# Optimization experiments

Hardware: AMD Instinct MI355X
Metric: run time of the kernel (lower is better)

Reference implementation:

```python
import jax, jax.numpy as jnp
import numpy as np

SAMPLERATE = 22050
N_OCTAVES = 16
N_SAMPLES = 32768
MIN_FREQ = 20.0 / (SAMPLERATE // 2)
MAX_FREQ = 3000.0 / (SAMPLERATE // 2)
FREQ_RANGE = MAX_FREQ - MIN_FREQ
BASE_RESONANCE = 0.01


def max_norm(x, axis=-1, eps=1e-8):
    return x / (jnp.max(jnp.abs(x), axis=axis, keepdims=True) + eps)


def exponential_decay(decay_values, n_octaves):
    # decay_values: (B, E, 1). Note the original applies sigmoid here on top of
    # the sigmoid already applied in forward (sigmoid_decay=True) -> double sigmoid.
    dv = jax.nn.sigmoid(decay_values)  # (B, E, 1)
    resonance_factor = (1.0 - BASE_RESONANCE) * 0.99
    decay = BASE_RESONANCE + dv * resonance_factor  # (B, E, 1)
    logd = jnp.log(decay + 1e-12)
    b, e, _ = decay_values.shape
    # cumsum of a per-(b,e) constant over octaves, then exp (matches torch code;
    # F.interpolate to size==n_octaves is the identity here)
    logd = jnp.broadcast_to(logd, (b, e, n_octaves))
    return jnp.exp(jnp.cumsum(logd, axis=-1))  # (B, E, O)


def setup_inputs() -> dict:
    key = jax.random.key(0)
    k1, k2, k3 = jax.random.split(key, 3)
    B, E = 8, 64
    return {
        "f0": jax.random.uniform(k1, (B, E, 1), dtype=jnp.float32),
        "decay_coefficients": jax.random.normal(k2, (B, E, 1), dtype=jnp.float32),
        "unused": jnp.zeros((B, E, 1), dtype=jnp.float32),
        "freq_spacing": jax.random.uniform(k3, (B, E, 1), dtype=jnp.float32),
    }


def reference(f0, decay_coefficients, unused, freq_spacing):
    b, e, _ = f0.shape
    O, S = N_OCTAVES, N_SAMPLES

    f0 = jnp.abs(f0)  # (B, E, 1)
    # sigmoid_decay=True path: sigmoid applied before exponential_decay
    exp_decays = exponential_decay(jax.nn.sigmoid(decay_coefficients), O)  # (B, E, O)

    f0 = (MIN_FREQ + f0 * FREQ_RANGE) * jnp.pi  # (B, E, 1)

    # freq_spacing repeated over octaves then cumsum -> per-octave factors
    factors = jnp.cumsum(jnp.broadcast_to(freq_spacing, (b, e, O)), axis=-1)
    f0s = f0 * factors  # (B, E, O)

    # nyquist cutoff
    f0s = f0s * (f0s < 1.0)

    # phase: cumsum over samples of constant per-octave frequency (faithful to torch)
    phase = jnp.cumsum(jnp.broadcast_to(f0s[..., None], (b, e, O, S)), axis=-1)
    osc = jnp.sin(phase)  # (B, E, O, S)

    osc = osc * exp_decays[..., None]
    osc = jnp.sum(osc, axis=2)  # (B, E, S)
    return max_norm(osc, axis=-1)
```

## Files before the change

### kernel.cpp

```cpp
#include <hip/hip_runtime.h>
#include <hip/hip_fp16.h>
#include <math.h>

#define N_OCT 16
#define NPAIR 8
#define NS    32768
#define TPB   512
#define SPT   (NS / TPB)
#define N_BE  512

typedef float v2f __attribute__((ext_vector_type(2)));
typedef _Float16 h4 __attribute__((ext_vector_type(4)));

static __device__ __forceinline__ v2f fma2(v2f a, v2f b, v2f c) {
    return __builtin_elementwise_fma(a, b, c);
}

__global__ __launch_bounds__(TPB, 4)
void f0res_kernel(const float* __restrict__ f0_in,
                  const float* __restrict__ dc_in,
                  const float* __restrict__ fs_in,
                  float* __restrict__ out)
{
    extern __shared__ _Float16 smem[];
    __shared__ float wmax[TPB / 64];

    const int be = blockIdx.x;
    const int t  = threadIdx.x;

    const float f0a = fabsf(f0_in[be]);
    const float dc  = dc_in[be];
    const float fs  = fs_in[be];

    const float MINF = (float)(20.0 / 11025.0);
    const float FRNG = (float)(3000.0 / 11025.0 - 20.0 / 11025.0);

    const float s1    = 1.0f / (1.0f + __expf(-dc));
    const float dv    = 1.0f / (1.0f + __expf(-s1));
    const float decay = 0.01f + dv * 0.9801f;
    const float logd  = __logf(decay + 1e-12f);
    const float f0r   = (MINF + f0a * FRNG) * 3.14159274101257324f;

    v2f xp[NPAIR], xc[NPAIR], c2h[NPAIR], c2l[NPAIR];

    float cl = 0.f, cf = 0.f;
    const double inv2pi = 0.15915494309189535;
    #pragma unroll
    for (int o = 0; o < N_OCT; ++o) {
        cl += logd;
        cf += fs;
        float ed  = __expf(cl);
        float f0s = f0r * cf;
        float a   = ed;
        if (!(f0s < 1.0f)) { a = 0.0f; f0s = 0.0f; }

        double r  = (double)f0s * inv2pi;
        double p0 = r * (double)(t + 1);
        p0 -= floor(p0);
        double pm = r * (double)(t + 1 - TPB);
        pm -= floor(pm);
        float xcur  = a * __builtin_amdgcn_sinf((float)p0);
        float xprev = a * __builtin_amdgcn_sinf((float)pm);

        double drev = r * (double)TPB;
        drev -= floor(drev);
        double c2d = 2.0 * cos(drev * 6.283185307179586);
        float  ch  = (float)c2d;
        float  clo = (float)(c2d - (double)ch);

        const int j = o >> 1;
        if ((o & 1) == 0) {
            xc[j].x = xcur;  xp[j].x = xprev;
            c2h[j].x = ch;   c2l[j].x = clo;
        } else {
            xc[j].y = xcur;  xp[j].y = xprev;
            c2h[j].y = ch;   c2l[j].y = clo;
        }
    }

    float lmax = 0.0f;
    #pragma unroll 4
    for (int k = 0; k < SPT; ++k) {
        v2f acc2 = (v2f)(0.0f);
        #pragma unroll
        for (int j = 0; j < NPAIR; ++j) {
            acc2 += xc[j];
            v2f xn = fma2(c2h[j], xc[j], fma2(c2l[j], xc[j], -xp[j]));
            xp[j] = xc[j];
            xc[j] = xn;
        }
        float acc = acc2.x + acc2.y;
        smem[k * TPB + t] = (_Float16)acc;
        lmax = fmaxf(lmax, fabsf(acc));
    }

    #pragma unroll
    for (int off = 32; off > 0; off >>= 1)
        lmax = fmaxf(lmax, __shfl_down(lmax, off, 64));
    if ((t & 63) == 0) wmax[t >> 6] = lmax;
    __syncthreads();
    float bmax = wmax[0];
    #pragma unroll
    for (int w = 1; w < TPB / 64; ++w) bmax = fmaxf(bmax, wmax[w]);

    const float norm = 1.0f / (bmax + 1e-8f);
    float4* out4 = (float4*)(out + (size_t)be * NS);
    #pragma unroll
    for (int j = 0; j < NS / 4 / TPB; ++j) {
        int i = j * TPB + t;
        h4 v = *(const h4*)(smem + 4 * (size_t)i);
        float4 o;
        o.x = (float)v.x * norm; o.y = (float)v.y * norm;
        o.z = (float)v.z * norm; o.w = (float)v.w * norm;
        out4[i] = o;
    }
}

extern "C" void kernel_launch(void* const* d_in, const int* in_sizes, int n_in,
                              void* d_out, int out_size, void* d_ws, size_t ws_size,
                              hipStream_t stream) {
    const float* f0 = (const float*)d_in[0];
    const float* dc = (const float*)d_in[1];
    const float* fs = (const float*)d_in[3];
    float* out = (float*)d_out;
    hipLaunchKernelGGL(f0res_kernel, dim3(N_BE), dim3(TPB),
                       NS * sizeof(_Float16), stream, f0, dc, fs, out);
}
```

Measured before the change: 109.6 us.

## Recompute oscillator bank in second pass instead of staging fp16 samples in LDS

Drops the 64KB fp16 shared-memory staging buffer and instead runs the recurrence twice: once to find the max, then again to write normalized fp32 output directly. Per-octave constants are now computed by 16 threads and shared through LDS rather than being computed redundantly by every thread. This removes LDS capacity pressure and the fp16 rounding, but doubles the recurrence arithmetic. Output stores become scalar per-thread strided writes instead of float4, and launch bounds change to 1 block per CU minimum.

```diff
diff --git a/kernel.cpp b/kernel.cpp
--- a/kernel.cpp
+++ b/kernel.cpp
@@ -1,5 +1,4 @@
 #include <hip/hip_runtime.h>
-#include <hip/hip_fp16.h>
 #include <math.h>
 
 #define N_OCT 16
@@ -10,74 +9,88 @@
 #define N_BE  512
 
 typedef float v2f __attribute__((ext_vector_type(2)));
-typedef _Float16 h4 __attribute__((ext_vector_type(4)));
 
 static __device__ __forceinline__ v2f fma2(v2f a, v2f b, v2f c) {
     return __builtin_elementwise_fma(a, b, c);
 }
 
-__global__ __launch_bounds__(TPB, 4)
-void f0res_kernel(const float* __restrict__ f0_in,
-                  const float* __restrict__ dc_in,
-                  const float* __restrict__ fs_in,
-                  float* __restrict__ out)
+__global__ __launch_bounds__(TPB, 1)
+void f0res_fused(const float* __restrict__ f0_in,
+                 const float* __restrict__ dc_in,
+                 const float* __restrict__ fs_in,
+                 float* __restrict__ out)
 {
-    extern __shared__ _Float16 smem[];
-    __shared__ float wmax[TPB / 64];
+    __shared__ double sh_r[N_OCT];
+    __shared__ float  sh_c2h[N_OCT], sh_c2l[N_OCT], sh_amp[N_OCT];
+    __shared__ float  wmax[TPB / 64];
 
     const int be = blockIdx.x;
     const int t  = threadIdx.x;
 
-    const float f0a = fabsf(f0_in[be]);
-    const float dc  = dc_in[be];
-    const float fs  = fs_in[be];
+    if (t < N_OCT) {
+        const int o = t;
+        const float f0a = fabsf(f0_in[be]);
+        const float dc  = dc_in[be];
+        const float fs  = fs_in[be];
 
-    const float MINF = (float)(20.0 / 11025.0);
-    const float FRNG = (float)(3000.0 / 11025.0 - 20.0 / 11025.0);
+        const float MINF = (float)(20.0 / 11025.0);
+        const float FRNG = (float)(3000.0 / 11025.0 - 20.0 / 11025.0);
 
-    const float s1    = 1.0f / (1.0f + __expf(-dc));
-    const float dv    = 1.0f / (1.0f + __expf(-s1));
-    const float decay = 0.01f + dv * 0.9801f;
-    const float logd  = __logf(decay + 1e-12f);
-    const float f0r   = (MINF + f0a * FRNG) * 3.14159274101257324f;
+        const float s1    = 1.0f / (1.0f + __expf(-dc));
+        const float dv    = 1.0f / (1.0f + __expf(-s1));
+        const float decay = 0.01f + dv * 0.9801f;
+        const float logd  = __logf(decay + 1e-12f);
+        const float f0r   = (MINF + f0a * FRNG) * 3.14159274101257324f;
 
-    v2f xp[NPAIR], xc[NPAIR], c2h[NPAIR], c2l[NPAIR];
-
-    float cl = 0.f, cf = 0.f;
-    const double inv2pi = 0.15915494309189535;
-    #pragma unroll
-    for (int o = 0; o < N_OCT; ++o) {
-        cl += logd;
-        cf += fs;
+        float cl = 0.f, cf = 0.f;
+        for (int i = 0; i <= o; ++i) { cl += logd; cf += fs; }
         float ed  = __expf(cl);
         float f0s = f0r * cf;
         float a   = ed;
         if (!(f0s < 1.0f)) { a = 0.0f; f0s = 0.0f; }
 
-        double r  = (double)f0s * inv2pi;
-        double p0 = r * (double)(t + 1);
-        p0 -= floor(p0);
-        double pm = r * (double)(t + 1 - TPB);
-        pm -= floor(pm);
-        float xcur  = a * __builtin_amdgcn_sinf((float)p0);
-        float xprev = a * __builtin_amdgcn_sinf((float)pm);
+        const double inv2pi = 0.15915494309189535;
+        double r = (double)f0s * inv2pi;
 
         double drev = r * (double)TPB;
         drev -= floor(drev);
         double c2d = 2.0 * cos(drev * 6.283185307179586);
         float  ch  = (float)c2d;
-        float  clo = (float)(c2d - (double)ch);
 
+        sh_r[o]   = r;
+        sh_c2h[o] = ch;
+        sh_c2l[o] = (float)(c2d - (double)ch);
+        sh_amp[o] = a;
+    }
+    __syncthreads();
+
+    v2f xp[NPAIR], xc[NPAIR], c2h[NPAIR], c2l[NPAIR];
+    #pragma unroll
+    for (int o = 0; o < N_OCT; ++o) {
         const int j = o >> 1;
-        if ((o & 1) == 0) {
-            xc[j].x = xcur;  xp[j].x = xprev;
-            c2h[j].x = ch;   c2l[j].x = clo;
-        } else {
-            xc[j].y = xcur;  xp[j].y = xprev;
-            c2h[j].y = ch;   c2l[j].y = clo;
-        }
+        float ch = sh_c2h[o], clo = sh_c2l[o];
+        if ((o & 1) == 0) { c2h[j].x = ch; c2l[j].x = clo; }
+        else              { c2h[j].y = ch; c2l[j].y = clo; }
     }
 
+    auto init_osc = [&]() {
+        #pragma unroll
+        for (int o = 0; o < N_OCT; ++o) {
+            const double r = sh_r[o];
+            const float  a = sh_amp[o];
+            double p0 = r * (double)(t + 1);
+            p0 -= floor(p0);
+            double pm = r * (double)(t + 1 - TPB);
+            pm -= floor(pm);
+            float xcur  = a * __builtin_amdgcn_sinf((float)p0);
+            float xprev = a * __builtin_amdgcn_sinf((float)pm);
+            const int j = o >> 1;
+            if ((o & 1) == 0) { xc[j].x = xcur; xp[j].x = xprev; }
+            else              { xc[j].y = xcur; xp[j].y = xprev; }
+        }
+    };
+
+    init_osc();
     float lmax = 0.0f;
     #pragma unroll 4
     for (int k = 0; k < SPT; ++k) {
@@ -89,9 +102,7 @@
             xp[j] = xc[j];
             xc[j] = xn;
         }
-        float acc = acc2.x + acc2.y;
-        smem[k * TPB + t] = (_Float16)acc;
-        lmax = fmaxf(lmax, fabsf(acc));
+        lmax = fmaxf(lmax, fabsf(acc2.x + acc2.y));
     }
 
     #pragma unroll
@@ -102,17 +113,21 @@
     float bmax = wmax[0];
     #pragma unroll
     for (int w = 1; w < TPB / 64; ++w) bmax = fmaxf(bmax, wmax[w]);
+    const float norm = 1.0f / (bmax + 1e-8f);
 
-    const float norm = 1.0f / (bmax + 1e-8f);
-    float4* out4 = (float4*)(out + (size_t)be * NS);
-    #pragma unroll
-    for (int j = 0; j < NS / 4 / TPB; ++j) {
-        int i = j * TPB + t;
-        h4 v = *(const h4*)(smem + 4 * (size_t)i);
-        float4 o;
-        o.x = (float)v.x * norm; o.y = (float)v.y * norm;
-        o.z = (float)v.z * norm; o.w = (float)v.w * norm;
-        out4[i] = o;
+    init_osc();
+    float* __restrict__ row = out + (size_t)be * NS;
+    #pragma unroll 4
+    for (int k = 0; k < SPT; ++k) {
+        v2f acc2 = (v2f)(0.0f);
+        #pragma unroll
+        for (int j = 0; j < NPAIR; ++j) {
+            acc2 += xc[j];
+            v2f xn = fma2(c2h[j], xc[j], fma2(c2l[j], xc[j], -xp[j]));
+            xp[j] = xc[j];
+            xc[j] = xn;
+        }
+        row[k * TPB + t] = (acc2.x + acc2.y) * norm;
     }
 }
 
@@ -123,6 +138,7 @@
     const float* dc = (const float*)d_in[1];
     const float* fs = (const float*)d_in[3];
     float* out = (float*)d_out;
-    hipLaunchKernelGGL(f0res_kernel, dim3(N_BE), dim3(TPB),
-                       NS * sizeof(_Float16), stream, f0, dc, fs, out);
+
+    hipLaunchKernelGGL(f0res_fused, dim3(N_BE), dim3(TPB), 0, stream,
+                       f0, dc, fs, out);
 }
```

Result: faster. 104.2 us (-4.9%).
